# Kernel optimization log

Measured on AMD Instinct MI355X. Metric: run time of the kernel, lower is better.

## Reference

```python
import jax, jax.numpy as jnp
import numpy as np

B, S, D, H = 8, 512, 1024, 16
DK = D // H          # 64
N_ASP = 4            # aspect tokens per sample
NEG = -1000000000.0


def setup_inputs() -> dict:
    key = jax.random.key(0)
    ks = jax.random.split(key, 12)
    return {
        "query": jax.random.normal(ks[0], (B, S, D), jnp.float32),
        "key_in": jax.random.normal(ks[1], (B, S, D), jnp.float32),
        "mask": jax.random.randint(ks[2], (B, S, S), 0, 2).astype(jnp.int32),
        "aspect": jax.random.normal(ks[3], (B, 1, D), jnp.float32),
        "aspect_ids": jax.random.randint(ks[4], (B, N_ASP), 0, S),
        # learned params
        "Wq": jax.random.normal(ks[5], (D, D), jnp.float32) / np.sqrt(D).astype(np.float32),
        "bq": jnp.zeros((D,), jnp.float32),
        "Wk": jax.random.normal(ks[6], (D, D), jnp.float32) / np.sqrt(D).astype(np.float32),
        "bk": jnp.zeros((D,), jnp.float32),
        "Wd": jax.random.normal(ks[7], (D, DK), jnp.float32) / np.sqrt(D).astype(np.float32),
        "bd": jnp.zeros((DK,), jnp.float32),
        "weight_m": jax.random.normal(ks[8], (H, DK, DK), jnp.float32) / np.sqrt(DK).astype(np.float32),
        "bias_m": jnp.zeros((1,), jnp.float32),
    }


def reference(query, key_in, mask, aspect, aspect_ids,
              Wq, bq, Wk, bk, Wd, bd, weight_m, bias_m):
    # projections -> [B,H,S,DK]
    q = (query @ Wq + bq).reshape(B, S, H, DK).transpose(0, 2, 1, 3)
    k = (key_in @ Wk + bk).reshape(B, S, H, DK).transpose(0, 2, 1, 3)

    # aspect -> dense -> broadcast to [B,H,S,DK]
    asp = aspect @ Wd + bd                                  # [B,1,DK]
    asp = jnp.broadcast_to(asp[:, None, :, :], (B, H, S, DK))

    # asps = tanh(aspect @ W_m @ K^T + bias_m)  -> [B,H,S,S]
    aw = jnp.einsum('bhsd,hde->bhse', asp, weight_m)
    asps = jnp.tanh(jnp.einsum('bhse,bhte->bhst', aw, k) + bias_m[0])

    # per-(batch,head) average score vector over rows -> [B,H,S]
    avg = asps.sum(axis=-2) / S

    # scatter: for each aspect index, overwrite its row and column with avg
    # (sequential over the small fixed N_ASP, matching torch write order:
    #  row write then column write per index)
    a_sc = asps
    bidx = jnp.arange(B)
    for j in range(N_ASP):
        idx = aspect_ids[:, j]                              # [B]
        a_sc = a_sc.at[bidx, :, idx, :].set(avg)            # rows
        a_sc = a_sc.at[bidx, :, :, idx].set(avg)            # cols

    # standard masked attention probs
    scores = jnp.einsum('bhsd,bhtd->bhst', q, k) / np.float32(np.sqrt(DK))
    scores = jnp.where(mask[:, None, :, :] == 0, NEG, scores)
    attn = jax.nn.softmax(scores, axis=-1)
    return a_sc, attn
```

## Files before the change

### kernel.cpp

```cpp
#include <hip/hip_runtime.h>

typedef __bf16 bf16x8 __attribute__((ext_vector_type(8)));
typedef float  f32x4  __attribute__((ext_vector_type(4)));

__device__ __forceinline__ unsigned short f2bf(float f) {
  union { float f; unsigned u; } x; x.f = f;
  unsigned r = (x.u + 0x7FFFu + ((x.u >> 16) & 1u)) >> 16;
  return (unsigned short)r;
}

__device__ __forceinline__ void gload_lds16(const void* g, void* l) {
  __builtin_amdgcn_global_load_lds((__attribute__((address_space(1))) void*)g,
                                   (__attribute__((address_space(3))) void*)l,
                                   16, 0, 0);
}

__global__ __launch_bounds__(256)
void prep_fused_kernel(const float* __restrict__ query, const float* __restrict__ key_in,
                       const float* __restrict__ Wq, const float* __restrict__ Wk,
                       const float* __restrict__ aspect, const float* __restrict__ Wd,
                       const float* __restrict__ bd, const float* __restrict__ weight_m,
                       const float* __restrict__ bk, const int* __restrict__ mask,
                       unsigned short* __restrict__ Aq, unsigned short* __restrict__ Ak,
                       unsigned short* __restrict__ Wqt, unsigned short* __restrict__ Wkt,
                       float* __restrict__ u_out, float* __restrict__ c_out,
                       unsigned long long* __restrict__ mb) {
  __shared__ __align__(16) char smem[2112];
  const int bx = blockIdx.x, tid = threadIdx.x;
  if (bx < 8192) {
    int i = bx * 256 + tid;
    if (i < 1048576) {
      float4 x = ((const float4*)query)[i];
      ushort4 y; y.x = f2bf(x.x); y.y = f2bf(x.y); y.z = f2bf(x.z); y.w = f2bf(x.w);
      ((ushort4*)Aq)[i] = y;
    } else {
      int j = i - 1048576;
      float4 x = ((const float4*)key_in)[j];
      ushort4 y; y.x = f2bf(x.x); y.y = f2bf(x.y); y.z = f2bf(x.z); y.w = f2bf(x.w);
      ((ushort4*)Ak)[j] = y;
    }
  } else if (bx < 10240) {
    int t = bx - 8192;
    const float* W = (t >> 10) ? Wk : Wq;
    unsigned short* Wt = (t >> 10) ? Wkt : Wqt;
    int tile_id = t & 1023;
    int k0 = (tile_id & 31) * 32, n0 = (tile_id >> 5) * 32;
    int tx = tid & 31, ty = tid >> 5;
    unsigned short (*tile)[33] = (unsigned short (*)[33])smem;
    #pragma unroll
    for (int i = 0; i < 4; ++i) {
      int k = ty + i * 8;
      tile[k][tx] = f2bf(W[(size_t)(k0 + k) * 1024 + n0 + tx]);
    }
    __syncthreads();
    #pragma unroll
    for (int i = 0; i < 4; ++i) {
      int n = ty + i * 8;
      Wt[(size_t)(n0 + n) * 1024 + k0 + tx] = tile[tx][n];
    }
  } else if (bx < 10496) {
    int t = bx - 10240;
    int gw = (t * 256 + tid) >> 6, lane = tid & 63;
    for (int row = gw; row < 4096; row += 1024) {
      const int* mr = mask + (size_t)row * 512;
      unsigned long long* dst = mb + (size_t)row * 8;
      #pragma unroll
      for (int it = 0; it < 8; ++it) {
        int m = mr[it * 64 + lane];
        unsigned long long bb = __ballot(m != 0);
        if (lane == 0) dst[it] = bb;
      }
    }
  } else {
    int id = bx - 10496;
    int bh = id >> 1, b = bh >> 4, h = bh & 15;
    int dbase = (id & 1) * 512;
    int e = tid & 63, g = tid >> 6;
    float* part  = (float*)smem;
    float* asp_s = part + 256;
    float* aw_s  = asp_s + 64;
    const float* arow = aspect + (size_t)b * 1024;
    float acc = 0.f;
    for (int d = g * 256; d < g * 256 + 256; ++d)
      acc += arow[d] * Wd[(size_t)d * 64 + e];
    part[g * 64 + e] = acc;
    __syncthreads();
    if (tid < 64)
      asp_s[tid] = bd[tid] + part[tid] + part[64 + tid] + part[128 + tid] + part[192 + tid];
    __syncthreads();
    if (tid < 64) {
      const float* wm = weight_m + (size_t)h * 4096;
      float aw = 0.f;
      #pragma unroll 8
      for (int d = 0; d < 64; ++d) aw += asp_s[d] * wm[d * 64 + tid];
      aw_s[tid] = aw;
    }
    __syncthreads();
    float awl = aw_s[e];
    if ((id & 1) == 0 && g == 0) {
      float s = bk[h * 64 + e] * awl;
      #pragma unroll
      for (int off = 32; off >= 1; off >>= 1) s += __shfl_xor(s, off, 64);
      if (e == 0) c_out[bh] = s;
    }
    const float* wkcol = Wk + h * 64 + e;
    #pragma unroll 2
    for (int it = 0; it < 32; ++it) {
      int d0 = dbase + g * 128 + it * 4;
      float s0 = wkcol[(size_t)d0 * 1024] * awl;
      float s1 = wkcol[(size_t)(d0 + 1) * 1024] * awl;
      float s2 = wkcol[(size_t)(d0 + 2) * 1024] * awl;
      float s3 = wkcol[(size_t)(d0 + 3) * 1024] * awl;
      #pragma unroll
      for (int off = 32; off >= 1; off >>= 1) {
        s0 += __shfl_xor(s0, off, 64);
        s1 += __shfl_xor(s1, off, 64);
        s2 += __shfl_xor(s2, off, 64);
        s3 += __shfl_xor(s3, off, 64);
      }
      if (e == 0) {
        float4 uo = {s0, s1, s2, s3};
        *(float4*)(u_out + (size_t)bh * 1024 + d0) = uo;
      }
    }
  }
}

__global__ __launch_bounds__(256)
void v_kernel(const float* __restrict__ key_in, const float* __restrict__ u,
              const float* __restrict__ c, const float* __restrict__ bias_m,
              float* __restrict__ v) {
  __shared__ float ks_[8][1024];
  int b = blockIdx.y, t0 = blockIdx.x * 8;
  int tid = threadIdx.x, wid = tid >> 6, lane = tid & 63;
  const float4* ksrc = (const float4*)(key_in + ((size_t)b * 512 + t0) * 1024);
  float4* kdst = (float4*)&ks_[0][0];
  for (int i = tid; i < 2048; i += 256) kdst[i] = ksrc[i];
  __syncthreads();
  const float* ub = u + (size_t)b * 16384;
  int r0 = wid * 2;
  float acc0[16] = {}, acc1[16] = {};
  for (int i = 0; i < 16; ++i) {
    int col = lane + 64 * i;
    float kv0 = ks_[r0][col], kv1 = ks_[r0 + 1][col];
    #pragma unroll
    for (int h = 0; h < 16; ++h) {
      float uv = ub[h * 1024 + col];
      acc0[h] += kv0 * uv;
      acc1[h] += kv1 * uv;
    }
  }
  float cb = bias_m[0];
  #pragma unroll
  for (int h = 0; h < 16; ++h) {
    float a0 = acc0[h], a1 = acc1[h];
    #pragma unroll
    for (int off = 32; off >= 1; off >>= 1) {
      a0 += __shfl_xor(a0, off, 64);
      a1 += __shfl_xor(a1, off, 64);
    }
    if (lane == h) {
      int bh = b * 16 + h;
      float cc = c[bh] + cb;
      v[(size_t)bh * 512 + t0 + r0]     = tanhf(a0 + cc);
      v[(size_t)bh * 512 + t0 + r0 + 1] = tanhf(a1 + cc);
    }
  }
}

__global__ void asc_kernel(const float* __restrict__ v, const int* __restrict__ ids,
                           float* __restrict__ out) {
  size_t i4 = (size_t)blockIdx.x * 256 + threadIdx.x;
  int t0 = (int)(i4 & 127) * 4;
  int s  = (int)(i4 >> 7) & 511;
  int bh = (int)(i4 >> 16);
  int b  = bh >> 4;
  int i0 = ids[b * 4], i1 = ids[b * 4 + 1], i2 = ids[b * 4 + 2], i3 = ids[b * 4 + 3];
  #define LASTOF(t) ((i3==(t))?3:(i2==(t))?2:(i1==(t))?1:(i0==(t))?0:-1)
  int ls  = LASTOF(s);
  int lt0 = LASTOF(t0), lt1 = LASTOF(t0+1), lt2 = LASTOF(t0+2), lt3 = LASTOF(t0+3);
  #undef LASTOF
  const float* vrow = v + (size_t)bh * 512;
  float vs = vrow[s];
  float4 vt = *(const float4*)(vrow + t0);
  f32x4 o;
  o[0] = (lt0 >= 0 && lt0 >= ls) ? vs : vt.x;
  o[1] = (lt1 >= 0 && lt1 >= ls) ? vs : vt.y;
  o[2] = (lt2 >= 0 && lt2 >= ls) ? vs : vt.z;
  o[3] = (lt3 >= 0 && lt3 >= ls) ? vs : vt.w;
  __builtin_nontemporal_store(o, ((f32x4*)out) + i4);
}

__global__ __launch_bounds__(256, 2)
void gemm_kernel(const unsigned short* __restrict__ Aq, const unsigned short* __restrict__ Ak,
                 const unsigned short* __restrict__ Bq, const unsigned short* __restrict__ Bk,
                 const float* __restrict__ bq, const float* __restrict__ bk,
                 unsigned short* __restrict__ qb, unsigned short* __restrict__ kb) {
  const unsigned short* A  = blockIdx.z ? Ak : Aq;
  const unsigned short* Bt = blockIdx.z ? Bk : Bq;
  const float* bias = blockIdx.z ? bk : bq;
  unsigned short* out = blockIdx.z ? kb : qb;
  const int m0 = blockIdx.x * 128, n0 = blockIdx.y * 128;
  __shared__ __align__(16) unsigned short As[128 * 64];
  __shared__ __align__(16) unsigned short Bs[128 * 64];
  const int tid = threadIdx.x, wid = tid >> 6, lane = tid & 63;
  const int wr = wid >> 1, wc = wid & 1;
  const int quad = lane >> 4, l15 = lane & 15;
  const int srw = lane >> 3;
  const int jcol = ((lane & 7) ^ srw) * 8;
  const int p0 = (quad ^ (l15 & 7)) * 8;
  f32x4 acc[4][4] = {};
  for (int k0 = 0; k0 < 1024; k0 += 64) {
    #pragma unroll
    for (int i = 0; i < 4; ++i) {
      int r = wid * 32 + i * 8 + srw;
      gload_lds16(A  + (size_t)(m0 + r) * 1024 + k0 + jcol, As + (wid * 32 + i * 8) * 64);
      gload_lds16(Bt + (size_t)(n0 + r) * 1024 + k0 + jcol, Bs + (wid * 32 + i * 8) * 64);
    }
    __syncthreads();
    bf16x8 af[4][2], bfr[4][2];
    #pragma unroll
    for (int mi = 0; mi < 4; ++mi) {
      const unsigned short* base = As + (wr * 64 + mi * 16 + l15) * 64;
      af[mi][0] = *(const bf16x8*)(base + p0);
      af[mi][1] = *(const bf16x8*)(base + (p0 ^ 32));
    }
    #pragma unroll
    for (int ni = 0; ni < 4; ++ni) {
      const unsigned short* base = Bs + (wc * 64 + ni * 16 + l15) * 64;
      bfr[ni][0] = *(const bf16x8*)(base + p0);
      bfr[ni][1] = *(const bf16x8*)(base + (p0 ^ 32));
    }
    #pragma unroll
    for (int mi = 0; mi < 4; ++mi)
      #pragma unroll
      for (int ni = 0; ni < 4; ++ni) {
        acc[mi][ni] = __builtin_amdgcn_mfma_f32_16x16x32_bf16(af[mi][0], bfr[ni][0], acc[mi][ni], 0, 0, 0);
        acc[mi][ni] = __builtin_amdgcn_mfma_f32_16x16x32_bf16(af[mi][1], bfr[ni][1], acc[mi][ni], 0, 0, 0);
      }
    __syncthreads();
  }
  #pragma unroll
  for (int mi = 0; mi < 4; ++mi) {
    #pragma unroll
    for (int ni = 0; ni < 4; ++ni) {
      const int n = n0 + wc * 64 + ni * 16 + l15;
      const int hh = n >> 6, dk = n & 63;
      const float bv = bias[n];
      #pragma unroll
      for (int r = 0; r < 4; ++r) {
        const int m = m0 + wr * 64 + mi * 16 + quad * 4 + r;
        const int bb = m >> 9, ss = m & 511;
        out[(((size_t)bb * 16 + hh) * 512 + ss) * 64 + dk] = f2bf(acc[mi][ni][r] + bv);
      }
    }
  }
}

__global__ __launch_bounds__(256, 2)
void attn_kernel(const unsigned short* __restrict__ qb, const unsigned short* __restrict__ kb,
                 const unsigned* __restrict__ mbits, float* __restrict__ attn) {
  __shared__ __align__(16) unsigned short ks[512 * 64];
  __shared__ __align__(16) unsigned short qs[64 * 64];
  const int bh = blockIdx.x, b = bh >> 4;
  const int s0 = blockIdx.y * 64;
  const int tid = threadIdx.x, wid = tid >> 6, lane = tid & 63;
  const int quad = lane >> 4, l15 = lane & 15;
  const int srw = lane >> 3;
  const int j8 = ((lane & 7) ^ srw) * 8;
  const int p0 = (quad ^ (l15 & 7)) * 8;
  const unsigned short* kslab = kb + (size_t)bh * 512 * 64;
  const unsigned short* qslab = qb + ((size_t)bh * 512 + s0) * 64;
  #pragma unroll
  for (int i = 0; i < 2; ++i)
    gload_lds16(qslab + (wid * 2 + i) * 512 + srw * 64 + j8, qs + (wid * 2 + i) * 512);
  #pragma unroll
  for (int i = 0; i < 16; ++i)
    gload_lds16(kslab + (wid * 16 + i) * 512 + srw * 64 + j8, ks + (wid * 16 + i) * 512);
  __syncthreads();
  const unsigned short* qbase = qs + (wid * 16 + l15) * 64;
  bf16x8 af0 = *(const bf16x8*)(qbase + p0);
  bf16x8 af1 = *(const bf16x8*)(qbase + (p0 ^ 32));
  f32x4 acc[32];
  #pragma unroll
  for (int tile = 0; tile < 32; ++tile) {
    const unsigned short* kbase = ks + (tile * 16 + l15) * 64;
    bf16x8 b0 = *(const bf16x8*)(kbase + p0);
    bf16x8 b1 = *(const bf16x8*)(kbase + (p0 ^ 32));
    f32x4 a = {0.f, 0.f, 0.f, 0.f};
    a = __builtin_amdgcn_mfma_f32_16x16x32_bf16(af0, b0, a, 0, 0, 0);
    a = __builtin_amdgcn_mfma_f32_16x16x32_bf16(af1, b1, a, 0, 0, 0);
    acc[tile] = a;
  }
  const size_t srow = (size_t)s0 + wid * 16 + quad * 4;
  const unsigned* mrow = mbits + ((size_t)b * 512 + srow) * 16;
  float mx[4] = {-3.0e38f, -3.0e38f, -3.0e38f, -3.0e38f};
  #pragma unroll
  for (int tp = 0; tp < 16; ++tp) {
    #pragma unroll
    for (int r = 0; r < 4; ++r) {
      unsigned m = mrow[(size_t)r * 16 + tp];
      float sc0 = acc[2 * tp][r] * 0.125f;
      float sc1 = acc[2 * tp + 1][r] * 0.125f;
      sc0 = ((m >> l15) & 1u) ? sc0 : -1.0e9f;
      sc1 = ((m >> (16 + l15)) & 1u) ? sc1 : -1.0e9f;
      acc[2 * tp][r] = sc0;
      acc[2 * tp + 1][r] = sc1;
      mx[r] = fmaxf(mx[r], fmaxf(sc0, sc1));
    }
  }
  #pragma unroll
  for (int r = 0; r < 4; ++r)
    #pragma unroll
    for (int off = 1; off < 16; off <<= 1)
      mx[r] = fmaxf(mx[r], __shfl_xor(mx[r], off, 64));
  float sm[4] = {0.f, 0.f, 0.f, 0.f};
  #pragma unroll
  for (int tile = 0; tile < 32; ++tile)
    #pragma unroll
    for (int r = 0; r < 4; ++r) {
      float e = __expf(acc[tile][r] - mx[r]);
      acc[tile][r] = e;
      sm[r] += e;
    }
  #pragma unroll
  for (int r = 0; r < 4; ++r) {
    #pragma unroll
    for (int off = 1; off < 16; off <<= 1)
      sm[r] += __shfl_xor(sm[r], off, 64);
    sm[r] = 1.0f / sm[r];
  }
  float* obase = attn + ((size_t)bh * 512 + srow) * 512 + l15;
  #pragma unroll
  for (int r = 0; r < 4; ++r)
    #pragma unroll
    for (int tile = 0; tile < 32; ++tile)
      __builtin_nontemporal_store(acc[tile][r] * sm[r], &obase[(size_t)r * 512 + tile * 16]);
}

extern "C" void kernel_launch(void* const* d_in, const int* in_sizes, int n_in,
                              void* d_out, int out_size, void* d_ws, size_t ws_size,
                              hipStream_t stream) {
  const float* query    = (const float*)d_in[0];
  const float* key_in   = (const float*)d_in[1];
  const int*   mask     = (const int*)d_in[2];
  const float* aspect   = (const float*)d_in[3];
  const int*   a_ids    = (const int*)d_in[4];
  const float* Wq       = (const float*)d_in[5];
  const float* bq       = (const float*)d_in[6];
  const float* Wk       = (const float*)d_in[7];
  const float* bk       = (const float*)d_in[8];
  const float* Wd       = (const float*)d_in[9];
  const float* bd       = (const float*)d_in[10];
  const float* weight_m = (const float*)d_in[11];
  const float* bias_m   = (const float*)d_in[12];

  float* out_asc  = (float*)d_out;
  float* out_attn = out_asc + 33554432ull;

  char* ws = (char*)d_ws;
  unsigned short* Aq   = (unsigned short*)(ws);
  unsigned short* Ak   = (unsigned short*)(ws + 8388608);
  unsigned short* Wqt  = (unsigned short*)(ws + 16777216);
  unsigned short* Wkt  = (unsigned short*)(ws + 18874368);
  unsigned short* qbuf = (unsigned short*)(ws + 20971520);
  unsigned short* kbuf = (unsigned short*)(ws + 29360128);
  float* u   = (float*)(ws + 37748736);
  float* c   = (float*)(ws + 38273024);
  float* v   = (float*)(ws + 38277120);
  unsigned long long* mb = (unsigned long long*)(ws + 38539264);

  prep_fused_kernel<<<dim3(10752), dim3(256), 0, stream>>>(
      query, key_in, Wq, Wk, aspect, Wd, bd, weight_m, bk, mask,
      Aq, Ak, Wqt, Wkt, u, c, mb);
  gemm_kernel<<<dim3(32, 8, 2), dim3(256), 0, stream>>>(Aq, Ak, Wqt, Wkt, bq, bk, qbuf, kbuf);
  v_kernel<<<dim3(64, 8), dim3(256), 0, stream>>>(key_in, u, c, bias_m, v);
  asc_kernel<<<dim3(32768), dim3(256), 0, stream>>>(v, a_ids, out_asc);
  attn_kernel<<<dim3(128, 8), dim3(256), 0, stream>>>(qbuf, kbuf, (const unsigned*)mb, out_attn);
}
```

Measured before the change: 464.3 us.

## Merge GEMM with v-kernel and attention with asc into combined launches

Folds the projection GEMM and the v computation into one launch, and the attention softmax and aspect-score scatter into another, by dispatching on block index. Small-work blocks in the prep kernel are reordered to run first. The attention path now reads K and Q straight from global memory instead of staging them in LDS, which frees shared memory and should raise occupancy, but K reuse now depends on cache. Launch count drops from five to three, cutting launch gaps and tail idle time.

Measured after the change: 431.1 us. 1.08x faster.

```diff
diff --git a/kernel.cpp b/kernel.cpp
--- a/kernel.cpp
+++ b/kernel.cpp
@@ -27,8 +27,8 @@
                        unsigned long long* __restrict__ mb) {
   __shared__ __align__(16) char smem[2112];
   const int bx = blockIdx.x, tid = threadIdx.x;
-  if (bx < 8192) {
-    int i = bx * 256 + tid;
+  if (bx >= 2560) {
+    int i = (bx - 2560) * 256 + tid;
     if (i < 1048576) {
       float4 x = ((const float4*)query)[i];
       ushort4 y; y.x = f2bf(x.x); y.y = f2bf(x.y); y.z = f2bf(x.z); y.w = f2bf(x.w);
@@ -39,8 +39,8 @@
       ushort4 y; y.x = f2bf(x.x); y.y = f2bf(x.y); y.z = f2bf(x.z); y.w = f2bf(x.w);
       ((ushort4*)Ak)[j] = y;
     }
-  } else if (bx < 10240) {
-    int t = bx - 8192;
+  } else if (bx >= 512) {
+    int t = bx - 512;
     const float* W = (t >> 10) ? Wk : Wq;
     unsigned short* Wt = (t >> 10) ? Wkt : Wqt;
     int tile_id = t & 1023;
@@ -58,8 +58,8 @@
       int n = ty + i * 8;
       Wt[(size_t)(n0 + n) * 1024 + k0 + tx] = tile[tx][n];
     }
-  } else if (bx < 10496) {
-    int t = bx - 10240;
+  } else if (bx >= 256) {
+    int t = bx - 256;
     int gw = (t * 256 + tid) >> 6, lane = tid & 63;
     for (int row = gw; row < 4096; row += 1024) {
       const int* mr = mask + (size_t)row * 512;
@@ -72,7 +72,7 @@
       }
     }
   } else {
-    int id = bx - 10496;
+    int id = bx;
     int bh = id >> 1, b = bh >> 4, h = bh & 15;
     int dbase = (id & 1) * 512;
     int e = tid & 63, g = tid >> 6;
@@ -126,216 +126,210 @@
   }
 }
 
-__global__ __launch_bounds__(256)
-void v_kernel(const float* __restrict__ key_in, const float* __restrict__ u,
-              const float* __restrict__ c, const float* __restrict__ bias_m,
-              float* __restrict__ v) {
-  __shared__ float ks_[8][1024];
-  int b = blockIdx.y, t0 = blockIdx.x * 8;
-  int tid = threadIdx.x, wid = tid >> 6, lane = tid & 63;
-  const float4* ksrc = (const float4*)(key_in + ((size_t)b * 512 + t0) * 1024);
-  float4* kdst = (float4*)&ks_[0][0];
-  for (int i = tid; i < 2048; i += 256) kdst[i] = ksrc[i];
-  __syncthreads();
-  const float* ub = u + (size_t)b * 16384;
-  int r0 = wid * 2;
-  float acc0[16] = {}, acc1[16] = {};
-  for (int i = 0; i < 16; ++i) {
-    int col = lane + 64 * i;
-    float kv0 = ks_[r0][col], kv1 = ks_[r0 + 1][col];
+__global__ __launch_bounds__(256, 2)
+void gemm_v_kernel(const unsigned short* __restrict__ Aq, const unsigned short* __restrict__ Ak,
+                   const unsigned short* __restrict__ Bq, const unsigned short* __restrict__ Bk,
+                   const float* __restrict__ bq, const float* __restrict__ bk,
+                   unsigned short* __restrict__ qb, unsigned short* __restrict__ kb,
+                   const float* __restrict__ key_in, const float* __restrict__ u,
+                   const float* __restrict__ c, const float* __restrict__ bias_m,
+                   float* __restrict__ v) {
+  __shared__ __align__(16) char smem[32768];
+  const int bx = blockIdx.x, tid = threadIdx.x;
+  if (bx < 512) {
+    const int z = bx >> 8;
+    const unsigned short* A  = z ? Ak : Aq;
+    const unsigned short* Bt = z ? Bk : Bq;
+    const float* bias = z ? bk : bq;
+    unsigned short* out = z ? kb : qb;
+    const int m0 = (bx & 31) * 128, n0 = ((bx >> 5) & 7) * 128;
+    unsigned short* As = (unsigned short*)smem;
+    unsigned short* Bs = (unsigned short*)(smem + 16384);
+    const int wid = tid >> 6, lane = tid & 63;
+    const int wr = wid >> 1, wc = wid & 1;
+    const int quad = lane >> 4, l15 = lane & 15;
+    const int srw = lane >> 3;
+    const int jcol = ((lane & 7) ^ srw) * 8;
+    const int p0 = (quad ^ (l15 & 7)) * 8;
+    f32x4 acc[4][4] = {};
+    for (int k0 = 0; k0 < 1024; k0 += 64) {
+      #pragma unroll
+      for (int i = 0; i < 4; ++i) {
+        int r = wid * 32 + i * 8 + srw;
+        gload_lds16(A  + (size_t)(m0 + r) * 1024 + k0 + jcol, As + (wid * 32 + i * 8) * 64);
+        gload_lds16(Bt + (size_t)(n0 + r) * 1024 + k0 + jcol, Bs + (wid * 32 + i * 8) * 64);
+      }
+      __syncthreads();
+      bf16x8 af[4][2], bfr[4][2];
+      #pragma unroll
+      for (int mi = 0; mi < 4; ++mi) {
+        const unsigned short* base = As + (wr * 64 + mi * 16 + l15) * 64;
+        af[mi][0] = *(const bf16x8*)(base + p0);
+        af[mi][1] = *(const bf16x8*)(base + (p0 ^ 32));
+      }
+      #pragma unroll
+      for (int ni = 0; ni < 4; ++ni) {
+        const unsigned short* base = Bs + (wc * 64 + ni * 16 + l15) * 64;
+        bfr[ni][0] = *(const bf16x8*)(base + p0);
+        bfr[ni][1] = *(const bf16x8*)(base + (p0 ^ 32));
+      }
+      #pragma unroll
+      for (int mi = 0; mi < 4; ++mi)
+        #pragma unroll
+        for (int ni = 0; ni < 4; ++ni) {
+          acc[mi][ni] = __builtin_amdgcn_mfma_f32_16x16x32_bf16(af[mi][0], bfr[ni][0], acc[mi][ni], 0, 0, 0);
+          acc[mi][ni] = __builtin_amdgcn_mfma_f32_16x16x32_bf16(af[mi][1], bfr[ni][1], acc[mi][ni], 0, 0, 0);
+        }
+      __syncthreads();
+    }
+    #pragma unroll
+    for (int mi = 0; mi < 4; ++mi) {
+      #pragma unroll
+      for (int ni = 0; ni < 4; ++ni) {
+        const int n = n0 + wc * 64 + ni * 16 + l15;
+        const int hh = n >> 6, dk = n & 63;
+        const float bv = bias[n];
+        #pragma unroll
+        for (int r = 0; r < 4; ++r) {
+          const int m = m0 + wr * 64 + mi * 16 + quad * 4 + r;
+          const int bb = m >> 9, ss = m & 511;
+          out[(((size_t)bb * 16 + hh) * 512 + ss) * 64 + dk] = f2bf(acc[mi][ni][r] + bv);
+        }
+      }
+    }
+  } else {
+    int vb = bx - 512;
+    int b = vb >> 6, t0 = (vb & 63) * 8;
+    int wid = tid >> 6, lane = tid & 63;
+    float (*ks_)[1024] = (float (*)[1024])smem;
+    const float4* ksrc = (const float4*)(key_in + ((size_t)b * 512 + t0) * 1024);
+    float4* kdst = (float4*)&ks_[0][0];
+    for (int i = tid; i < 2048; i += 256) kdst[i] = ksrc[i];
+    __syncthreads();
+    const float* ub = u + (size_t)b * 16384;
+    int r0 = wid * 2;
+    float acc0[16] = {}, acc1[16] = {};
+    for (int i = 0; i < 16; ++i) {
+      int col = lane + 64 * i;
+      float kv0 = ks_[r0][col], kv1 = ks_[r0 + 1][col];
+      #pragma unroll
+      for (int h = 0; h < 16; ++h) {
+        float uv = ub[h * 1024 + col];
+        acc0[h] += kv0 * uv;
+        acc1[h] += kv1 * uv;
+      }
+    }
+    float cb = bias_m[0];
     #pragma unroll
     for (int h = 0; h < 16; ++h) {
-      float uv = ub[h * 1024 + col];
-      acc0[h] += kv0 * uv;
-      acc1[h] += kv1 * uv;
+      float a0 = acc0[h], a1 = acc1[h];
+      #pragma unroll
+      for (int off = 32; off >= 1; off >>= 1) {
+        a0 += __shfl_xor(a0, off, 64);
+        a1 += __shfl_xor(a1, off, 64);
+      }
+      if (lane == h) {
+        int bh = b * 16 + h;
+        float cc = c[bh] + cb;
+        v[(size_t)bh * 512 + t0 + r0]     = tanhf(a0 + cc);
+        v[(size_t)bh * 512 + t0 + r0 + 1] = tanhf(a1 + cc);
+      }
     }
   }
-  float cb = bias_m[0];
-  #pragma unroll
-  for (int h = 0; h < 16; ++h) {
-    float a0 = acc0[h], a1 = acc1[h];
-    #pragma unroll
-    for (int off = 32; off >= 1; off >>= 1) {
-      a0 += __shfl_xor(a0, off, 64);
-      a1 += __shfl_xor(a1, off, 64);
-    }
-    if (lane == h) {
-      int bh = b * 16 + h;
-      float cc = c[bh] + cb;
-      v[(size_t)bh * 512 + t0 + r0]     = tanhf(a0 + cc);
-      v[(size_t)bh * 512 + t0 + r0 + 1] = tanhf(a1 + cc);
-    }
+}
+
+__global__ __launch_bounds__(256, 2)
+void attn_asc_kernel(const unsigned short* __restrict__ qb, const unsigned short* __restrict__ kb,
+                     const unsigned* __restrict__ mbits, const float* __restrict__ vv,
+                     const int* __restrict__ ids, float* __restrict__ attn,
+                     float* __restrict__ out_asc) {
+  const int bx = blockIdx.x, tid = threadIdx.x;
+  if (bx < 1024) {
+    const int bh = bx & 127, b = bh >> 4;
+    const int s0 = (bx >> 7) * 64;
+    const int wid = tid >> 6, lane = tid & 63;
+    const int quad = lane >> 4, l15 = lane & 15;
+    const unsigned short* kslab = kb + (size_t)bh * 512 * 64;
+    const unsigned short* qslab = qb + ((size_t)bh * 512 + s0) * 64;
+    const unsigned short* qptr = qslab + (wid * 16 + l15) * 64 + quad * 8;
+    bf16x8 af0 = *(const bf16x8*)(qptr);
+    bf16x8 af1 = *(const bf16x8*)(qptr + 32);
+    const unsigned short* kptr = kslab + l15 * 64 + quad * 8;
+    f32x4 acc[32];
+    #pragma unroll
+    for (int tile = 0; tile < 32; ++tile) {
+      bf16x8 b0 = *(const bf16x8*)(kptr + tile * 1024);
+      bf16x8 b1 = *(const bf16x8*)(kptr + tile * 1024 + 32);
+      f32x4 a = {0.f, 0.f, 0.f, 0.f};
+      a = __builtin_amdgcn_mfma_f32_16x16x32_bf16(af0, b0, a, 0, 0, 0);
+      a = __builtin_amdgcn_mfma_f32_16x16x32_bf16(af1, b1, a, 0, 0, 0);
+      acc[tile] = a;
+    }
+    const size_t srow = (size_t)s0 + wid * 16 + quad * 4;
+    const unsigned* mrow = mbits + ((size_t)b * 512 + srow) * 16;
+    float mx[4] = {-3.0e38f, -3.0e38f, -3.0e38f, -3.0e38f};
+    #pragma unroll
+    for (int tp = 0; tp < 16; ++tp) {
+      #pragma unroll
+      for (int r = 0; r < 4; ++r) {
+        unsigned m = mrow[(size_t)r * 16 + tp];
+        float sc0 = acc[2 * tp][r] * 0.125f;
+        float sc1 = acc[2 * tp + 1][r] * 0.125f;
+        sc0 = ((m >> l15) & 1u) ? sc0 : -1.0e9f;
+        sc1 = ((m >> (16 + l15)) & 1u) ? sc1 : -1.0e9f;
+        acc[2 * tp][r] = sc0;
+        acc[2 * tp + 1][r] = sc1;
+        mx[r] = fmaxf(mx[r], fmaxf(sc0, sc1));
+      }
+    }
+    #pragma unroll
+    for (int r = 0; r < 4; ++r)
+      #pragma unroll
+      for (int off = 1; off < 16; off <<= 1)
+        mx[r] = fmaxf(mx[r], __shfl_xor(mx[r], off, 64));
+    float sm[4] = {0.f, 0.f, 0.f, 0.f};
+    #pragma unroll
+    for (int tile = 0; tile < 32; ++tile)
+      #pragma unroll
+      for (int r = 0; r < 4; ++r) {
+        float e = __expf(acc[tile][r] - mx[r]);
+        acc[tile][r] = e;
+        sm[r] += e;
+      }
+    #pragma unroll
+    for (int r = 0; r < 4; ++r) {
+      #pragma unroll
+      for (int off = 1; off < 16; off <<= 1)
+        sm[r] += __shfl_xor(sm[r], off, 64);
+      sm[r] = 1.0f / sm[r];
+    }
+    float* obase = attn + ((size_t)bh * 512 + srow) * 512 + l15;
+    #pragma unroll
+    for (int r = 0; r < 4; ++r)
+      #pragma unroll
+      for (int tile = 0; tile < 32; ++tile)
+        __builtin_nontemporal_store(acc[tile][r] * sm[r], &obase[(size_t)r * 512 + tile * 16]);
+  } else {
+    size_t i4 = (size_t)(bx - 1024) * 256 + tid;
+    int t0 = (int)(i4 & 127) * 4;
+    int s  = (int)(i4 >> 7) & 511;
+    int bh = (int)(i4 >> 16);
+    int b  = bh >> 4;
+    int i0 = ids[b * 4], i1 = ids[b * 4 + 1], i2 = ids[b * 4 + 2], i3 = ids[b * 4 + 3];
+    #define LASTOF(t) ((i3==(t))?3:(i2==(t))?2:(i1==(t))?1:(i0==(t))?0:-1)
+    int ls  = LASTOF(s);
+    int lt0 = LASTOF(t0), lt1 = LASTOF(t0+1), lt2 = LASTOF(t0+2), lt3 = LASTOF(t0+3);
+    #undef LASTOF
+    const float* vrow = vv + (size_t)bh * 512;
+    float vs = vrow[s];
+    float4 vt = *(const float4*)(vrow + t0);
+    f32x4 o;
+    o[0] = (lt0 >= 0 && lt0 >= ls) ? vs : vt.x;
+    o[1] = (lt1 >= 0 && lt1 >= ls) ? vs : vt.y;
+    o[2] = (lt2 >= 0 && lt2 >= ls) ? vs : vt.z;
+    o[3] = (lt3 >= 0 && lt3 >= ls) ? vs : vt.w;
+    __builtin_nontemporal_store(o, ((f32x4*)out_asc) + i4);
   }
-}
-
-__global__ void asc_kernel(const float* __restrict__ v, const int* __restrict__ ids,
-                           float* __restrict__ out) {
-  size_t i4 = (size_t)blockIdx.x * 256 + threadIdx.x;
-  int t0 = (int)(i4 & 127) * 4;
-  int s  = (int)(i4 >> 7) & 511;
-  int bh = (int)(i4 >> 16);
-  int b  = bh >> 4;
-  int i0 = ids[b * 4], i1 = ids[b * 4 + 1], i2 = ids[b * 4 + 2], i3 = ids[b * 4 + 3];
-  #define LASTOF(t) ((i3==(t))?3:(i2==(t))?2:(i1==(t))?1:(i0==(t))?0:-1)
-  int ls  = LASTOF(s);
-  int lt0 = LASTOF(t0), lt1 = LASTOF(t0+1), lt2 = LASTOF(t0+2), lt3 = LASTOF(t0+3);
-  #undef LASTOF
-  const float* vrow = v + (size_t)bh * 512;
-  float vs = vrow[s];
-  float4 vt = *(const float4*)(vrow + t0);
-  f32x4 o;
-  o[0] = (lt0 >= 0 && lt0 >= ls) ? vs : vt.x;
-  o[1] = (lt1 >= 0 && lt1 >= ls) ? vs : vt.y;
-  o[2] = (lt2 >= 0 && lt2 >= ls) ? vs : vt.z;
-  o[3] = (lt3 >= 0 && lt3 >= ls) ? vs : vt.w;
-  __builtin_nontemporal_store(o, ((f32x4*)out) + i4);
-}
-
-__global__ __launch_bounds__(256, 2)
-void gemm_kernel(const unsigned short* __restrict__ Aq, const unsigned short* __restrict__ Ak,
-                 const unsigned short* __restrict__ Bq, const unsigned short* __restrict__ Bk,
-                 const float* __restrict__ bq, const float* __restrict__ bk,
-                 unsigned short* __restrict__ qb, unsigned short* __restrict__ kb) {
-  const unsigned short* A  = blockIdx.z ? Ak : Aq;
-  const unsigned short* Bt = blockIdx.z ? Bk : Bq;
-  const float* bias = blockIdx.z ? bk : bq;
-  unsigned short* out = blockIdx.z ? kb : qb;
-  const int m0 = blockIdx.x * 128, n0 = blockIdx.y * 128;
-  __shared__ __align__(16) unsigned short As[128 * 64];
-  __shared__ __align__(16) unsigned short Bs[128 * 64];
-  const int tid = threadIdx.x, wid = tid >> 6, lane = tid & 63;
-  const int wr = wid >> 1, wc = wid & 1;
-  const int quad = lane >> 4, l15 = lane & 15;
-  const int srw = lane >> 3;
-  const int jcol = ((lane & 7) ^ srw) * 8;
-  const int p0 = (quad ^ (l15 & 7)) * 8;
-  f32x4 acc[4][4] = {};
-  for (int k0 = 0; k0 < 1024; k0 += 64) {
-    #pragma unroll
-    for (int i = 0; i < 4; ++i) {
-      int r = wid * 32 + i * 8 + srw;
-      gload_lds16(A  + (size_t)(m0 + r) * 1024 + k0 + jcol, As + (wid * 32 + i * 8) * 64);
-      gload_lds16(Bt + (size_t)(n0 + r) * 1024 + k0 + jcol, Bs + (wid * 32 + i * 8) * 64);
-    }
-    __syncthreads();
-    bf16x8 af[4][2], bfr[4][2];
-    #pragma unroll
-    for (int mi = 0; mi < 4; ++mi) {
-      const unsigned short* base = As + (wr * 64 + mi * 16 + l15) * 64;
-      af[mi][0] = *(const bf16x8*)(base + p0);
-      af[mi][1] = *(const bf16x8*)(base + (p0 ^ 32));
-    }
-    #pragma unroll
-    for (int ni = 0; ni < 4; ++ni) {
-      const unsigned short* base = Bs + (wc * 64 + ni * 16 + l15) * 64;
-      bfr[ni][0] = *(const bf16x8*)(base + p0);
-      bfr[ni][1] = *(const bf16x8*)(base + (p0 ^ 32));
-    }
-    #pragma unroll
-    for (int mi = 0; mi < 4; ++mi)
-      #pragma unroll
-      for (int ni = 0; ni < 4; ++ni) {
-        acc[mi][ni] = __builtin_amdgcn_mfma_f32_16x16x32_bf16(af[mi][0], bfr[ni][0], acc[mi][ni], 0, 0, 0);
-        acc[mi][ni] = __builtin_amdgcn_mfma_f32_16x16x32_bf16(af[mi][1], bfr[ni][1], acc[mi][ni], 0, 0, 0);
-      }
-    __syncthreads();
-  }
-  #pragma unroll
-  for (int mi = 0; mi < 4; ++mi) {
-    #pragma unroll
-    for (int ni = 0; ni < 4; ++ni) {
-      const int n = n0 + wc * 64 + ni * 16 + l15;
-      const int hh = n >> 6, dk = n & 63;
-      const float bv = bias[n];
-      #pragma unroll
-      for (int r = 0; r < 4; ++r) {
-        const int m = m0 + wr * 64 + mi * 16 + quad * 4 + r;
-        const int bb = m >> 9, ss = m & 511;
-        out[(((size_t)bb * 16 + hh) * 512 + ss) * 64 + dk] = f2bf(acc[mi][ni][r] + bv);
-      }
-    }
-  }
-}
-
-__global__ __launch_bounds__(256, 2)
-void attn_kernel(const unsigned short* __restrict__ qb, const unsigned short* __restrict__ kb,
-                 const unsigned* __restrict__ mbits, float* __restrict__ attn) {
-  __shared__ __align__(16) unsigned short ks[512 * 64];
-  __shared__ __align__(16) unsigned short qs[64 * 64];
-  const int bh = blockIdx.x, b = bh >> 4;
-  const int s0 = blockIdx.y * 64;
-  const int tid = threadIdx.x, wid = tid >> 6, lane = tid & 63;
-  const int quad = lane >> 4, l15 = lane & 15;
-  const int srw = lane >> 3;
-  const int j8 = ((lane & 7) ^ srw) * 8;
-  const int p0 = (quad ^ (l15 & 7)) * 8;
-  const unsigned short* kslab = kb + (size_t)bh * 512 * 64;
-  const unsigned short* qslab = qb + ((size_t)bh * 512 + s0) * 64;
-  #pragma unroll
-  for (int i = 0; i < 2; ++i)
-    gload_lds16(qslab + (wid * 2 + i) * 512 + srw * 64 + j8, qs + (wid * 2 + i) * 512);
-  #pragma unroll
-  for (int i = 0; i < 16; ++i)
-    gload_lds16(kslab + (wid * 16 + i) * 512 + srw * 64 + j8, ks + (wid * 16 + i) * 512);
-  __syncthreads();
-  const unsigned short* qbase = qs + (wid * 16 + l15) * 64;
-  bf16x8 af0 = *(const bf16x8*)(qbase + p0);
-  bf16x8 af1 = *(const bf16x8*)(qbase + (p0 ^ 32));
-  f32x4 acc[32];
-  #pragma unroll
-  for (int tile = 0; tile < 32; ++tile) {
-    const unsigned short* kbase = ks + (tile * 16 + l15) * 64;
-    bf16x8 b0 = *(const bf16x8*)(kbase + p0);
-    bf16x8 b1 = *(const bf16x8*)(kbase + (p0 ^ 32));
-    f32x4 a = {0.f, 0.f, 0.f, 0.f};
-    a = __builtin_amdgcn_mfma_f32_16x16x32_bf16(af0, b0, a, 0, 0, 0);
-    a = __builtin_amdgcn_mfma_f32_16x16x32_bf16(af1, b1, a, 0, 0, 0);
-    acc[tile] = a;
-  }
-  const size_t srow = (size_t)s0 + wid * 16 + quad * 4;
-  const unsigned* mrow = mbits + ((size_t)b * 512 + srow) * 16;
-  float mx[4] = {-3.0e38f, -3.0e38f, -3.0e38f, -3.0e38f};
-  #pragma unroll
-  for (int tp = 0; tp < 16; ++tp) {
-    #pragma unroll
-    for (int r = 0; r < 4; ++r) {
-      unsigned m = mrow[(size_t)r * 16 + tp];
-      float sc0 = acc[2 * tp][r] * 0.125f;
-      float sc1 = acc[2 * tp + 1][r] * 0.125f;
-      sc0 = ((m >> l15) & 1u) ? sc0 : -1.0e9f;
-      sc1 = ((m >> (16 + l15)) & 1u) ? sc1 : -1.0e9f;
-      acc[2 * tp][r] = sc0;
-      acc[2 * tp + 1][r] = sc1;
-      mx[r] = fmaxf(mx[r], fmaxf(sc0, sc1));
-    }
-  }
-  #pragma unroll
-  for (int r = 0; r < 4; ++r)
-    #pragma unroll
-    for (int off = 1; off < 16; off <<= 1)
-      mx[r] = fmaxf(mx[r], __shfl_xor(mx[r], off, 64));
-  float sm[4] = {0.f, 0.f, 0.f, 0.f};
-  #pragma unroll
-  for (int tile = 0; tile < 32; ++tile)
-    #pragma unroll
-    for (int r = 0; r < 4; ++r) {
-      float e = __expf(acc[tile][r] - mx[r]);
-      acc[tile][r] = e;
-      sm[r] += e;
-    }
-  #pragma unroll
-  for (int r = 0; r < 4; ++r) {
-    #pragma unroll
-    for (int off = 1; off < 16; off <<= 1)
-      sm[r] += __shfl_xor(sm[r], off, 64);
-    sm[r] = 1.0f / sm[r];
-  }
-  float* obase = attn + ((size_t)bh * 512 + srow) * 512 + l15;
-  #pragma unroll
-  for (int r = 0; r < 4; ++r)
-    #pragma unroll
-    for (int tile = 0; tile < 32; ++tile)
-      __builtin_nontemporal_store(acc[tile][r] * sm[r], &obase[(size_t)r * 512 + tile * 16]);
 }
 
 extern "C" void kernel_launch(void* const* d_in, const int* in_sizes, int n_in,
@@ -373,8 +367,8 @@
   prep_fused_kernel<<<dim3(10752), dim3(256), 0, stream>>>(
       query, key_in, Wq, Wk, aspect, Wd, bd, weight_m, bk, mask,
       Aq, Ak, Wqt, Wkt, u, c, mb);
-  gemm_kernel<<<dim3(32, 8, 2), dim3(256), 0, stream>>>(Aq, Ak, Wqt, Wkt, bq, bk, qbuf, kbuf);
-  v_kernel<<<dim3(64, 8), dim3(256), 0, stream>>>(key_in, u, c, bias_m, v);
-  asc_kernel<<<dim3(32768), dim3(256), 0, stream>>>(v, a_ids, out_asc);
-  attn_kernel<<<dim3(128, 8), dim3(256), 0, stream>>>(qbuf, kbuf, (const unsigned*)mb, out_attn);
-}
+  gemm_v_kernel<<<dim3(1024), dim3(256), 0, stream>>>(
+      Aq, Ak, Wqt, Wkt, bq, bk, qbuf, kbuf, key_in, u, c, bias_m, v);
+  attn_asc_kernel<<<dim3(33792), dim3(256), 0, stream>>>(
+      qbuf, kbuf, (const unsigned*)mb, v, a_ids, out_attn, out_asc);
+}
```
